# Optimization experiments

Measured on AMD Instinct MI355X. Metric: run time of the kernel, lower is better.

The kernel has to match this reference:

```python
import jax, jax.numpy as jnp
import numpy as np
import math

B, S, DIM = 2, 2048, 4096
N_HEADS, N_KV_HEADS = 32, 8
HEAD_DIM = DIM // N_HEADS  # 128
N_REP = N_HEADS // N_KV_HEADS  # 4
ROPE_THETA = 10000.0


def setup_inputs() -> dict:
    key = jax.random.key(0)
    ks = jax.random.split(key, 6)
    x = jax.random.normal(ks[0], (B, S, DIM), dtype=jnp.float32)
    wq = jax.random.normal(ks[1], (DIM, DIM), dtype=jnp.float32) * 0.02
    wk = jax.random.normal(ks[2], (N_KV_HEADS * HEAD_DIM, DIM), dtype=jnp.float32) * 0.02
    wv = jax.random.normal(ks[3], (N_KV_HEADS * HEAD_DIM, DIM), dtype=jnp.float32) * 0.02
    wo = jax.random.normal(ks[4], (DIM, DIM), dtype=jnp.float32) * 0.02
    # rotary freqs_cis (seqlen, head_dim//2), represented as cos/sin
    inv_freq = 1.0 / (ROPE_THETA ** (jnp.arange(0, HEAD_DIM, 2, dtype=jnp.float32) / HEAD_DIM))
    angles = jnp.arange(S, dtype=jnp.float32)[:, None] * inv_freq[None, :]  # [S, HEAD_DIM//2]
    freqs_cos = jnp.cos(angles)
    freqs_sin = jnp.sin(angles)
    # additive causal mask [S, S]: 0 on/below diagonal, -inf above
    mask = jnp.where(jnp.tril(jnp.ones((S, S), dtype=bool)), 0.0, -jnp.inf).astype(jnp.float32)
    return {"x": x, "wq": wq, "wk": wk, "wv": wv, "wo": wo,
            "freqs_cos": freqs_cos, "freqs_sin": freqs_sin, "mask": mask}


def _apply_rotary(t, freqs_cos, freqs_sin):
    # t: [B, S, H, HEAD_DIM]; interpret pairs (even, odd) as complex
    t2 = t.reshape(*t.shape[:-1], HEAD_DIM // 2, 2)
    tr, ti = t2[..., 0], t2[..., 1]
    c = freqs_cos[None, :, None, :]  # [1, S, 1, HD/2]
    s = freqs_sin[None, :, None, :]
    out_r = tr * c - ti * s
    out_i = tr * s + ti * c
    return jnp.stack([out_r, out_i], axis=-1).reshape(t.shape)


def reference(x, wq, wk, wv, wo, freqs_cos, freqs_sin, mask):
    bsz, seqlen, _ = x.shape
    xq = (x @ wq.T).reshape(bsz, seqlen, N_HEADS, HEAD_DIM)
    xk = (x @ wk.T).reshape(bsz, seqlen, N_KV_HEADS, HEAD_DIM)
    xv = (x @ wv.T).reshape(bsz, seqlen, N_KV_HEADS, HEAD_DIM)
    xq = _apply_rotary(xq, freqs_cos, freqs_sin)
    xk = _apply_rotary(xk, freqs_cos, freqs_sin)
    # repeat_kv (GQA): [B,S,KV,HD] -> [B,S,KV*N_REP,HD] via repeat_interleave on head axis
    keys = jnp.repeat(xk, N_REP, axis=2)
    values = jnp.repeat(xv, N_REP, axis=2)
    # scores: [B, H, S, S]
    scores = jnp.einsum('bqhd,bkhd->bhqk', xq, keys) / math.sqrt(HEAD_DIM)
    scores = scores + mask[None, None, :, :]
    probs = jax.nn.softmax(scores.astype(jnp.float32), axis=-1).astype(xq.dtype)
    out = jnp.einsum('bhqk,bkhd->bqhd', probs, values).reshape(bsz, seqlen, DIM)
    return out @ wo.T
```

## Files before the change

### kernel.cpp

```cpp
#include <hip/hip_runtime.h>

typedef __bf16 bf16;
typedef __bf16 bf16x4 __attribute__((ext_vector_type(4)));
typedef __bf16 bf16x8 __attribute__((ext_vector_type(8)));
typedef float f32x4 __attribute__((ext_vector_type(4)));

#define BB 2
#define SS 2048
#define DIM 4096
#define KVDIM 1024
#define NH 32
#define NKV 8
#define HD 128
#define NEGINF (-1e30f)

__device__ __forceinline__ void async16(void* lds, const void* gmem) {
    __builtin_amdgcn_global_load_lds(
        (const __attribute__((address_space(1))) void*)gmem,
        (__attribute__((address_space(3))) void*)lds, 16, 0, 0);
}

__device__ __forceinline__ f32x4 mfma16(bf16x8 a, bf16x8 b, f32x4 c) {
    return __builtin_amdgcn_mfma_f32_16x16x32_bf16(a, b, c, 0, 0, 0);
}

struct DetectArgs { const void* p[7]; int n[7]; };

__global__ void detect_dtypes(DetectArgs a, int* flags) {
    __shared__ int bad;
    const int ti = blockIdx.x;
    if (threadIdx.x == 0) bad = 0;
    __syncthreads();
    const bf16* s = (const bf16*)a.p[ti];
    int n = a.n[ti];
    int take = n < 8192 ? n : 8192;
    int lbad = 0;
    for (int i = threadIdx.x; i < take; i += 256) {
        float f = (float)s[i];
        if (!(f > -1e4f && f < 1e4f)) lbad = 1;
    }
    if (lbad) atomicOr(&bad, 1);
    __syncthreads();
    if (threadIdx.x == 0) flags[ti] = bad;
}

__device__ __forceinline__ void conv8(const void* src, bf16* dst, int rel, int flag) {
    if (flag) {
        const float* s = (const float*)src + (size_t)rel * 8;
        bf16x8 v;
#pragma unroll
        for (int j = 0; j < 8; ++j) v[j] = (bf16)s[j];
        *(bf16x8*)(dst + (size_t)rel * 8) = v;
    } else {
        *(bf16x8*)(dst + (size_t)rel * 8) = *((const bf16x8*)src + rel);
    }
}

__global__ void convert_to_bf16(const void* __restrict__ src, bf16* __restrict__ dst,
                                int n8, const int* __restrict__ flagp) {
    int i = blockIdx.x * 256 + threadIdx.x;
    if (i >= n8) return;
    conv8(src, dst, i, *flagp);
}

__global__ void convert4(const void* s0, bf16* d0, int n0, const int* f0,
                         const void* s1, bf16* d1, int n1, const int* f1,
                         const void* s2, bf16* d2, int n2, const int* f2,
                         const void* s3, bf16* d3, int n3, const int* f3) {
    int u = blockIdx.x * 256 + threadIdx.x;
    if (u < n0)                       { conv8(s0, d0, u, *f0); return; }
    u -= n0;
    if (u < n1)                       { conv8(s1, d1, u, *f1); return; }
    u -= n1;
    if (u < n2)                       { conv8(s2, d2, u, *f2); return; }
    u -= n2;
    if (u < n3)                       { conv8(s3, d3, u, *f3); return; }
}

#define SBAR()  asm volatile("s_barrier" ::: "memory")
#define LGKM0() asm volatile("s_waitcnt lgkmcnt(0)" ::: "memory")
#define VM8()   asm volatile("s_waitcnt vmcnt(8)" ::: "memory")
#define VM4()   asm volatile("s_waitcnt vmcnt(4)" ::: "memory")
#define VM0()   asm volatile("s_waitcnt vmcnt(0)" ::: "memory")

__device__ __forceinline__ void gemm256_core(const bf16* __restrict__ A,
                                             const bf16* __restrict__ B,
                                             int K, int m0, int n0,
                                             f32x4 (&acc)[8][4]) {
    __shared__ bf16 sm[2][4][8192];
    const int t = threadIdx.x;
    const int lane = t & 63;
    const int w = t >> 6;
    const int l15 = lane & 15, quad = lane >> 4;
    const int wm = w >> 2;
    const int wn = w & 3;
    const int axr = l15 & 7;
    const int c0 = (quad ^ axr) * 8;
    const int c1 = ((4 + quad) ^ axr) * 8;
    const int srl = t >> 3;
    const int sch = ((t & 7) ^ (srl & 7)) * 8;
    const size_t Ks = (size_t)K;

    bf16x8 aReg[4][2], bReg[4][2];

#define RD_A(c_, mh) { \
    const bf16* ab = &sm[c_][wm][0] + ((mh) * 64 + l15) * 64; \
    _Pragma("unroll") for (int i = 0; i < 4; ++i) { \
        aReg[i][0] = *(const bf16x8*)(ab + i * 1024 + c0); \
        aReg[i][1] = *(const bf16x8*)(ab + i * 1024 + c1); } }

#define RD_B(c_, nh) { \
    const bf16* bb = &sm[c_][2 + (wn >> 1)][0] + ((wn & 1) * 64 + (nh) * 32 + l15) * 64; \
    _Pragma("unroll") for (int jj = 0; jj < 2; ++jj) { \
        bReg[(nh) * 2 + jj][0] = *(const bf16x8*)(bb + jj * 1024 + c0); \
        bReg[(nh) * 2 + jj][1] = *(const bf16x8*)(bb + jj * 1024 + c1); } }

#define STG(c_, reg_, Mat, rowbase, kt) { \
    bf16* d_ = &sm[c_][reg_][0] + (size_t)t * 8; \
    const bf16* s_ = (Mat) + ((size_t)((rowbase) + srl)) * Ks + (size_t)(kt) * 64 + sch; \
    async16(d_, s_); \
    async16(d_ + 4096, s_ + 64 * Ks); }

#define MM(mh, nh) { \
    _Pragma("unroll") for (int i = 0; i < 4; ++i) \
    _Pragma("unroll") for (int jj = 0; jj < 2; ++jj) { \
        acc[(mh) * 4 + i][(nh) * 2 + jj] = \
            mfma16(aReg[i][0], bReg[(nh) * 2 + jj][0], acc[(mh) * 4 + i][(nh) * 2 + jj]); \
        acc[(mh) * 4 + i][(nh) * 2 + jj] = \
            mfma16(aReg[i][1], bReg[(nh) * 2 + jj][1], acc[(mh) * 4 + i][(nh) * 2 + jj]); } }

    STG(0, 0, A, m0, 0);
    STG(0, 2, B, n0, 0);
    STG(0, 1, A, m0 + 128, 0);
    STG(0, 3, B, n0 + 128, 0);
    STG(1, 2, B, n0, 1);
    STG(1, 0, A, m0, 1);
    VM4(); SBAR();

    const int NT = K >> 6;
    for (int T = 0; T < NT; ++T) {
        const int c = T & 1, nc = c ^ 1;
        const int kt1 = (T + 1 < NT) ? T + 1 : 0;
        const int kt2 = (T + 2 < NT) ? T + 2 : 0;
        RD_A(c, 0); RD_B(c, 0);
        STG(nc, 1, A, m0 + 128, kt1);
        SBAR();
        __builtin_amdgcn_s_setprio(1); MM(0, 0); __builtin_amdgcn_s_setprio(0);
        LGKM0(); SBAR();
        RD_B(c, 1);
        STG(nc, 3, B, n0 + 128, kt1);
        SBAR();
        __builtin_amdgcn_s_setprio(1); MM(0, 1); __builtin_amdgcn_s_setprio(0);
        LGKM0(); SBAR();
        RD_A(c, 1);
        STG(c, 2, B, n0, kt2);
        SBAR();
        __builtin_amdgcn_s_setprio(1); MM(1, 0); __builtin_amdgcn_s_setprio(0);
        LGKM0(); SBAR();
        STG(c, 0, A, m0, kt2);
        SBAR();
        __builtin_amdgcn_s_setprio(1); MM(1, 1); __builtin_amdgcn_s_setprio(0);
        LGKM0(); VM4(); SBAR();
    }
#undef RD_A
#undef RD_B
#undef STG
#undef MM
}

__global__ __launch_bounds__(512, 2)
void gemm_nt(const bf16* __restrict__ A, const bf16* __restrict__ B,
             bf16* __restrict__ C, int M, int N, int K) {
    const int t = threadIdx.x, lane = t & 63, w = t >> 6;
    const int l15 = lane & 15, quad = lane >> 4;
    const int wm = w >> 2, wn = w & 3;
    const int m0 = blockIdx.y * 256, n0 = blockIdx.x * 256;
    f32x4 acc[8][4] = {};
    gemm256_core(A, B, K, m0, n0, acc);
#pragma unroll
    for (int i = 0; i < 8; ++i)
#pragma unroll
        for (int j = 0; j < 4; ++j) {
            int col = n0 + wn * 64 + j * 16 + l15;
#pragma unroll
            for (int r = 0; r < 4; ++r)
                C[(size_t)(m0 + wm * 128 + i * 16 + quad * 4 + r) * N + col] = (bf16)acc[i][j][r];
        }
}

__global__ __launch_bounds__(512, 2)
void gemm_nt_kv(const bf16* __restrict__ A, const bf16* __restrict__ Bkv,
                bf16* __restrict__ Kc, bf16* __restrict__ Vc, int M, int K) {
    const int t = threadIdx.x, lane = t & 63, w = t >> 6;
    const int l15 = lane & 15, quad = lane >> 4;
    const int wm = w >> 2, wn = w & 3;
    const int m0 = blockIdx.y * 256, n0 = blockIdx.x * 256;
    f32x4 acc[8][4] = {};
    gemm256_core(A, Bkv, K, m0, n0, acc);
    bf16* C = (n0 < KVDIM) ? Kc : Vc;
    const int cb = (n0 < KVDIM) ? n0 : n0 - KVDIM;
#pragma unroll
    for (int i = 0; i < 8; ++i)
#pragma unroll
        for (int j = 0; j < 4; ++j) {
            int col = cb + wn * 64 + j * 16 + l15;
#pragma unroll
            for (int r = 0; r < 4; ++r)
                C[(size_t)(m0 + wm * 128 + i * 16 + quad * 4 + r) * KVDIM + col] = (bf16)acc[i][j][r];
        }
}

__global__ __launch_bounds__(512, 2)
void gemm_nt_out(const bf16* __restrict__ A, const bf16* __restrict__ B,
                 void* __restrict__ C, int M, int N, int K,
                 const int* __restrict__ flagp) {
    const int t = threadIdx.x, lane = t & 63, w = t >> 6;
    const int l15 = lane & 15, quad = lane >> 4;
    const int wm = w >> 2, wn = w & 3;
    const int m0 = blockIdx.y * 256, n0 = blockIdx.x * 256;
    const int f32out = *flagp;
    f32x4 acc[8][4] = {};
    gemm256_core(A, B, K, m0, n0, acc);
#pragma unroll
    for (int i = 0; i < 8; ++i)
#pragma unroll
        for (int j = 0; j < 4; ++j) {
            int col = n0 + wn * 64 + j * 16 + l15;
#pragma unroll
            for (int r = 0; r < 4; ++r) {
                int row = m0 + wm * 128 + i * 16 + quad * 4 + r;
                if (f32out) ((float*)C)[(size_t)row * N + col] = acc[i][j][r];
                else        ((bf16*)C)[(size_t)row * N + col] = (bf16)acc[i][j][r];
            }
        }
}

__device__ __forceinline__ void rope8(bf16* p, const bf16* fc, const bf16* fs,
                                      int s, int i0, float sc) {
    bf16x8 v = *(bf16x8*)p;
    bf16x8 o;
#pragma unroll
    for (int j = 0; j < 4; ++j) {
        float tr = (float)v[2 * j], ti = (float)v[2 * j + 1];
        float cc = (float)fc[s * 64 + i0 + j];
        float sn = (float)fs[s * 64 + i0 + j];
        o[2 * j]     = (bf16)((tr * cc - ti * sn) * sc);
        o[2 * j + 1] = (bf16)((tr * sn + ti * cc) * sc);
    }
    *(bf16x8*)p = o;
}

#define ROPE_BLOCKS ((DIM * (BB * SS) / 8 + KVDIM * (BB * SS) / 8) / 256)

__global__ void rope_tv(bf16* __restrict__ Q, bf16* __restrict__ Kr,
                        const bf16* __restrict__ fc, const bf16* __restrict__ fs,
                        const bf16* __restrict__ V, bf16* __restrict__ Vt) {
    __shared__ bf16 tile[64][74];
    const int bid = blockIdx.x;
    const int t = threadIdx.x;
    if (bid < ROPE_BLOCKS) {
        const float qscale = 0.08838834764831845f * 1.4426950408889634f;
        int u = bid * 256 + t;
        const int QU = (DIM * (BB * SS)) / 8;
        if (u < QU) {
            int row = u >> 9;
            int c = (u & 511) * 8;
            rope8(Q + (size_t)row * DIM + c, fc, fs, row & (SS - 1), (c >> 1) & 63, qscale);
        } else {
            u -= QU;
            int row = u >> 7;
            int c = (u & 127) * 8;
            rope8(Kr + (size_t)row * KVDIM + c, fc, fs, row & (SS - 1), (c >> 1) & 63, 1.0f);
        }
        return;
    }
    const int b2 = bid - ROPE_BLOCKS;
    const int st = b2 & 31, ct = (b2 >> 5) & 15, b = b2 >> 9;
    const int s0 = st * 64;
    const int kvh = ct >> 1, d0 = (ct & 1) * 64;
#pragma unroll
    for (int i = 0; i < 2; ++i) {
        int o = i * 256 + t;
        int r = o >> 3, c8 = (o & 7) * 8;
        bf16x8 v = *(const bf16x8*)(V + (size_t)(b * SS + s0 + r) * KVDIM + kvh * HD + d0 + c8);
#pragma unroll
        for (int j = 0; j < 8; ++j) tile[r][c8 + j] = v[j];
    }
    __syncthreads();
#pragma unroll
    for (int i = 0; i < 2; ++i) {
        int o = i * 256 + t;
        int sseg = (o & 7) * 8, dl = o >> 3;
        bf16x8 v;
#pragma unroll
        for (int j = 0; j < 8; ++j) v[j] = tile[sseg + j][dl];
        *(bf16x8*)(Vt + ((size_t)((b * NKV + kvh) * HD) + d0 + dl) * SS + s0 + sseg) = v;
    }
}

__global__ __launch_bounds__(256, 2)
void flash_attn(const bf16* __restrict__ Q, const bf16* __restrict__ Kr,
                const bf16* __restrict__ Vt, bf16* __restrict__ AO) {
    __shared__ char smem[49152];
    bf16* Vts = (bf16*)(smem + 32768);
    const int t = threadIdx.x, w = t >> 6, lane = t & 63;
    const int l15 = lane & 15, quad = lane >> 4;
    const int bh = blockIdx.x;
    const int b = bh >> 5, h = bh & 31, kvh = h >> 2;
    const int q0 = ((int)gridDim.y - 1 - (int)blockIdx.y) * 128;

#define STAGE_K(kb_, kk_) { \
    char* kbase_ = smem + (kb_) * 16384; \
    _Pragma("unroll") for (int i = 0; i < 4; ++i) { \
        int s_ = i * 256 + t; \
        int key_ = s_ >> 4, slot_ = s_ & 15; \
        int dseg_ = slot_ ^ (key_ & 15); \
        async16(kbase_ + (size_t)s_ * 16, \
                Kr + (size_t)(b * SS + (kk_) + key_) * KVDIM + kvh * HD + dseg_ * 8); } }
#define STAGE_V(kk_) { \
    _Pragma("unroll") for (int i = 0; i < 4; ++i) { \
        int s_ = i * 256 + t; \
        int d_ = s_ >> 3, slot_ = s_ & 7; \
        int kseg_ = slot_ ^ (d_ & 7); \
        async16((char*)Vts + (size_t)s_ * 16, \
                Vt + ((size_t)((b * NKV + kvh) * HD + d_)) * SS + (kk_) + kseg_ * 8); } }

    bf16x8 qf[2][4];
#pragma unroll
    for (int mi = 0; mi < 2; ++mi) {
        int qrow = b * SS + q0 + w * 32 + mi * 16 + l15;
#pragma unroll
        for (int ks = 0; ks < 4; ++ks)
            qf[mi][ks] = *(const bf16x8*)(Q + (size_t)qrow * DIM + h * HD + ks * 32 + quad * 8);
    }

    f32x4 of[2][8] = {};
    float mrow[2] = {NEGINF, NEGINF};
    float lrow[2] = {0.f, 0.f};

    const int nt = (q0 + 128) >> 6;
    STAGE_K(0, 0);
    for (int ti = 0; ti < nt; ++ti) {
        const int kk = ti << 6;
        const int cur = ti & 1, nxt = cur ^ 1;
        bf16* Ks = (bf16*)(smem + cur * 16384);
        char* Ps = smem + cur * 16384;
        STAGE_V(kk);
        STAGE_K(nxt, (ti + 1 < nt) ? kk + 64 : 0);
        VM8(); SBAR();

        f32x4 sacc[2][4] = {};
#pragma unroll
        for (int nt2 = 0; nt2 < 4; ++nt2) {
            int key = nt2 * 16 + l15;
#pragma unroll
            for (int ks = 0; ks < 4; ++ks) {
                int slot = (ks * 4 + quad) ^ (key & 15);
                bf16x8 kf = *(const bf16x8*)(Ks + key * 128 + slot * 8);
#pragma unroll
                for (int mi = 0; mi < 2; ++mi)
                    sacc[mi][nt2] = mfma16(kf, qf[mi][ks], sacc[mi][nt2]);
            }
        }
        if (kk >= q0) {
#pragma unroll
            for (int mi = 0; mi < 2; ++mi) {
                int q = q0 + w * 32 + mi * 16 + l15;
#pragma unroll
                for (int nt2 = 0; nt2 < 4; ++nt2) {
                    int kbase = kk + nt2 * 16 + quad * 4;
#pragma unroll
                    for (int r = 0; r < 4; ++r)
                        if (kbase + r > q) sacc[mi][nt2][r] = NEGINF;
                }
            }
        }
#pragma unroll
        for (int mi = 0; mi < 2; ++mi) {
            float m01[4];
#pragma unroll
            for (int nt2 = 0; nt2 < 4; ++nt2)
                m01[nt2] = fmaxf(fmaxf(sacc[mi][nt2][0], sacc[mi][nt2][1]),
                                 fmaxf(sacc[mi][nt2][2], sacc[mi][nt2][3]));
            float mx = fmaxf(fmaxf(m01[0], m01[1]), fmaxf(m01[2], m01[3]));
            mx = fmaxf(mx, __shfl_xor(mx, 16));
            mx = fmaxf(mx, __shfl_xor(mx, 32));
            if (__all(mx - mrow[mi] <= 8.0f)) {
                float rs[4];
#pragma unroll
                for (int nt2 = 0; nt2 < 4; ++nt2) {
                    rs[nt2] = 0.f;
#pragma unroll
                    for (int r = 0; r < 4; ++r) {
                        float p = exp2f(sacc[mi][nt2][r] - mrow[mi]);
                        sacc[mi][nt2][r] = p;
                        rs[nt2] += p;
                    }
                }
                float rsum = (rs[0] + rs[1]) + (rs[2] + rs[3]);
                rsum += __shfl_xor(rsum, 16);
                rsum += __shfl_xor(rsum, 32);
                lrow[mi] += rsum;
            } else {
                float mnew = fmaxf(mrow[mi], mx);
                float alpha = exp2f(mrow[mi] - mnew);
                float rs[4];
#pragma unroll
                for (int nt2 = 0; nt2 < 4; ++nt2) {
                    rs[nt2] = 0.f;
#pragma unroll
                    for (int r = 0; r < 4; ++r) {
                        float p = exp2f(sacc[mi][nt2][r] - mnew);
                        sacc[mi][nt2][r] = p;
                        rs[nt2] += p;
                    }
                }
                float rsum = (rs[0] + rs[1]) + (rs[2] + rs[3]);
                rsum += __shfl_xor(rsum, 16);
                rsum += __shfl_xor(rsum, 32);
                lrow[mi] = lrow[mi] * alpha + rsum;
                mrow[mi] = mnew;
#pragma unroll
                for (int dt = 0; dt < 8; ++dt)
#pragma unroll
                    for (int r = 0; r < 4; ++r) of[mi][dt][r] *= alpha;
            }
        }
        VM4(); SBAR();
#pragma unroll
        for (int mi = 0; mi < 2; ++mi) {
            int row = w * 32 + mi * 16 + l15;
#pragma unroll
            for (int nt2 = 0; nt2 < 4; ++nt2) {
                bf16x4 pv;
#pragma unroll
                for (int r = 0; r < 4; ++r) pv[r] = (bf16)sacc[mi][nt2][r];
                int cc = nt2 * 2 + (quad >> 1);
                *(bf16x4*)(Ps + row * 128 + ((cc ^ (row & 7)) * 16 + (quad & 1) * 8)) = pv;
            }
        }
#pragma unroll
        for (int kb = 0; kb < 2; ++kb) {
            bf16x8 pa[2];
#pragma unroll
            for (int mi = 0; mi < 2; ++mi) {
                int row = w * 32 + mi * 16 + l15;
                pa[mi] = *(const bf16x8*)(Ps + row * 128 + (((kb * 4 + quad) ^ (row & 7)) * 16));
            }
#pragma unroll
            for (int dt = 0; dt < 8; ++dt) {
                int d = dt * 16 + l15;
                int slot = (kb * 4 + quad) ^ (d & 7);
                bf16x8 vb = *(const bf16x8*)(Vts + d * 64 + slot * 8);
#pragma unroll
                for (int mi = 0; mi < 2; ++mi)
                    of[mi][dt] = mfma16(vb, pa[mi], of[mi][dt]);
            }
        }
        SBAR();
    }
    VM0(); SBAR();
#undef STAGE_K
#undef STAGE_V
    bf16* Os = (bf16*)smem;
#pragma unroll
    for (int mi = 0; mi < 2; ++mi) {
        float inv = 1.0f / lrow[mi];
        int row = w * 32 + mi * 16 + l15;
#pragma unroll
        for (int dt = 0; dt < 8; ++dt) {
            bf16x4 o4;
#pragma unroll
            for (int r = 0; r < 4; ++r) o4[r] = (bf16)(of[mi][dt][r] * inv);
            int s = dt * 2 + (quad >> 1);
            int slot = s ^ l15;
            *(bf16x4*)((char*)Os + row * 256 + slot * 16 + (quad & 1) * 8) = o4;
        }
    }
    __syncthreads();
#pragma unroll
    for (int i = 0; i < 8; ++i) {
        int flat = i * 256 + t;
        int ql = flat >> 4, s = flat & 15;
        bf16x8 v = *(const bf16x8*)((char*)Os + ql * 256 + (s ^ (ql & 15)) * 16);
        *(bf16x8*)(AO + (size_t)(b * SS + q0 + ql) * DIM + h * HD + s * 8) = v;
    }
}

extern "C" void kernel_launch(void* const* d_in, const int* in_sizes, int n_in,
                              void* d_out, int out_size, void* d_ws, size_t ws_size,
                              hipStream_t stream) {
    const size_t MD = (size_t)BB * SS * DIM;
    const size_t KV = (size_t)BB * SS * KVDIM;
    const size_t FC = (size_t)SS * (HD / 2);
    const int M = BB * SS;

    int* flags = (int*)d_ws;
    bf16* xb  = (bf16*)((char*)d_ws + 32);
    bf16* wb  = xb + MD;
    bf16* Q   = wb + MD;
    bf16* Kr  = Q + MD;
    bf16* Vw  = Kr + KV;
    bf16* Vt  = Vw + KV;
    bf16* fcb = Vt + KV;
    bf16* fsb = fcb + FC;

    DetectArgs da;
    for (int i = 0; i < 7; ++i) { da.p[i] = d_in[i]; da.n[i] = in_sizes[i]; }
    detect_dtypes<<<7, 256, 0, stream>>>(da, flags);

    dim3 blk(256);
    dim3 blk512(512);

    {
        int n0 = (int)(MD / 8), n1 = (int)(FC / 8), n2 = (int)(FC / 8), n3 = (int)(MD / 8);
        int nb = (n0 + n1 + n2 + n3 + 255) / 256;
        convert4<<<nb, blk, 0, stream>>>(d_in[0], xb, n0, flags + 0,
                                         d_in[5], fcb, n1, flags + 5,
                                         d_in[6], fsb, n2, flags + 6,
                                         d_in[1], wb, n3, flags + 1);
    }
    gemm_nt<<<dim3(DIM / 256, M / 256), blk512, 0, stream>>>(xb, wb, Q, M, DIM, DIM);

    {
        int n0 = (int)(KV / 8), n1 = (int)(KV / 8);
        int nb = (n0 + n1 + 255) / 256;
        convert4<<<nb, blk, 0, stream>>>(d_in[2], wb, n0, flags + 2,
                                         d_in[3], wb + KV, n1, flags + 3,
                                         nullptr, nullptr, 0, flags + 2,
                                         nullptr, nullptr, 0, flags + 2);
    }
    gemm_nt_kv<<<dim3(2 * KVDIM / 256, M / 256), blk512, 0, stream>>>(xb, wb, Kr, Vw, M, DIM);

    rope_tv<<<dim3(ROPE_BLOCKS + (SS / 64) * 16 * BB), blk, 0, stream>>>(Q, Kr, fcb, fsb, Vw, Vt);

    flash_attn<<<dim3(BB * NH, SS / 128), blk, 0, stream>>>(Q, Kr, Vt, xb);

    convert_to_bf16<<<(int)(MD / 8 / 256), blk, 0, stream>>>(d_in[4], wb, (int)(MD / 8), flags + 4);
    gemm_nt_out<<<dim3(DIM / 256, M / 256), blk512, 0, stream>>>(xb, wb, d_out, M, DIM, DIM, flags + 0);
}
```

Before: 727.7 us.

## Widen flash attention blocks to 256 queries with 8 waves sharing K/V tiles

The flash attention kernel now runs 512 threads over 256 query rows per block instead of 256 threads over 128 rows. Each K/V tile staged in LDS is therefore reused by twice as many waves, which halves global K/V traffic per query. K double-buffering is dropped: each iteration loads K and V, then waits before computing, so load latency is no longer hidden behind compute. A per-wave 'live' flag skips QK, softmax and PV work on tiles that lie entirely above the causal diagonal. The epilogue writes the output in two halves to fit LDS. Risks are exposed load latency, waves sitting idle at barriers on causal-edge tiles, and fewer blocks in the grid.

```diff
diff --git a/kernel.cpp b/kernel.cpp
--- a/kernel.cpp
+++ b/kernel.cpp
@@ -79,8 +79,8 @@
 
 #define SBAR()  asm volatile("s_barrier" ::: "memory")
 #define LGKM0() asm volatile("s_waitcnt lgkmcnt(0)" ::: "memory")
-#define VM8()   asm volatile("s_waitcnt vmcnt(8)" ::: "memory")
 #define VM4()   asm volatile("s_waitcnt vmcnt(4)" ::: "memory")
+#define VM2()   asm volatile("s_waitcnt vmcnt(2)" ::: "memory")
 #define VM0()   asm volatile("s_waitcnt vmcnt(0)" ::: "memory")
 
 __device__ __forceinline__ void gemm256_core(const bf16* __restrict__ A,
@@ -298,28 +298,30 @@
     }
 }
 
-__global__ __launch_bounds__(256, 2)
+__global__ __launch_bounds__(512, 2)
 void flash_attn(const bf16* __restrict__ Q, const bf16* __restrict__ Kr,
                 const bf16* __restrict__ Vt, bf16* __restrict__ AO) {
     __shared__ char smem[49152];
+    bf16* Ks  = (bf16*)smem;
+    char* Ps  = smem;
     bf16* Vts = (bf16*)(smem + 32768);
     const int t = threadIdx.x, w = t >> 6, lane = t & 63;
     const int l15 = lane & 15, quad = lane >> 4;
     const int bh = blockIdx.x;
     const int b = bh >> 5, h = bh & 31, kvh = h >> 2;
-    const int q0 = ((int)gridDim.y - 1 - (int)blockIdx.y) * 128;
-
-#define STAGE_K(kb_, kk_) { \
-    char* kbase_ = smem + (kb_) * 16384; \
-    _Pragma("unroll") for (int i = 0; i < 4; ++i) { \
-        int s_ = i * 256 + t; \
+    const int q0 = ((int)gridDim.y - 1 - (int)blockIdx.y) * 256;
+    const int qw = q0 + w * 32;
+
+#define STAGE_K(kk_) { \
+    _Pragma("unroll") for (int i = 0; i < 2; ++i) { \
+        int s_ = i * 512 + t; \
         int key_ = s_ >> 4, slot_ = s_ & 15; \
         int dseg_ = slot_ ^ (key_ & 15); \
-        async16(kbase_ + (size_t)s_ * 16, \
+        async16((char*)Ks + (size_t)s_ * 16, \
                 Kr + (size_t)(b * SS + (kk_) + key_) * KVDIM + kvh * HD + dseg_ * 8); } }
 #define STAGE_V(kk_) { \
-    _Pragma("unroll") for (int i = 0; i < 4; ++i) { \
-        int s_ = i * 256 + t; \
+    _Pragma("unroll") for (int i = 0; i < 2; ++i) { \
+        int s_ = i * 512 + t; \
         int d_ = s_ >> 3, slot_ = s_ & 7; \
         int kseg_ = slot_ ^ (d_ & 7); \
         async16((char*)Vts + (size_t)s_ * 16, \
@@ -328,7 +330,7 @@
     bf16x8 qf[2][4];
 #pragma unroll
     for (int mi = 0; mi < 2; ++mi) {
-        int qrow = b * SS + q0 + w * 32 + mi * 16 + l15;
+        int qrow = b * SS + qw + mi * 16 + l15;
 #pragma unroll
         for (int ks = 0; ks < 4; ++ks)
             qf[mi][ks] = *(const bf16x8*)(Q + (size_t)qrow * DIM + h * HD + ks * 32 + quad * 8);
@@ -338,152 +340,157 @@
     float mrow[2] = {NEGINF, NEGINF};
     float lrow[2] = {0.f, 0.f};
 
-    const int nt = (q0 + 128) >> 6;
-    STAGE_K(0, 0);
-    for (int ti = 0; ti < nt; ++ti) {
-        const int kk = ti << 6;
-        const int cur = ti & 1, nxt = cur ^ 1;
-        bf16* Ks = (bf16*)(smem + cur * 16384);
-        char* Ps = smem + cur * 16384;
+    const int kend = q0 + 256;
+    for (int kk = 0; kk < kend; kk += 64) {
+        STAGE_K(kk);
         STAGE_V(kk);
-        STAGE_K(nxt, (ti + 1 < nt) ? kk + 64 : 0);
-        VM8(); SBAR();
-
+        VM2(); SBAR();
+
+        const bool live = kk <= qw + 31;
         f32x4 sacc[2][4] = {};
-#pragma unroll
-        for (int nt2 = 0; nt2 < 4; ++nt2) {
-            int key = nt2 * 16 + l15;
-#pragma unroll
-            for (int ks = 0; ks < 4; ++ks) {
-                int slot = (ks * 4 + quad) ^ (key & 15);
-                bf16x8 kf = *(const bf16x8*)(Ks + key * 128 + slot * 8);
-#pragma unroll
-                for (int mi = 0; mi < 2; ++mi)
-                    sacc[mi][nt2] = mfma16(kf, qf[mi][ks], sacc[mi][nt2]);
-            }
-        }
-        if (kk >= q0) {
+        if (live) {
+#pragma unroll
+            for (int nt2 = 0; nt2 < 4; ++nt2) {
+                int key = nt2 * 16 + l15;
+#pragma unroll
+                for (int ks = 0; ks < 4; ++ks) {
+                    int slot = (ks * 4 + quad) ^ (key & 15);
+                    bf16x8 kf = *(const bf16x8*)(Ks + key * 128 + slot * 8);
+#pragma unroll
+                    for (int mi = 0; mi < 2; ++mi)
+                        sacc[mi][nt2] = mfma16(kf, qf[mi][ks], sacc[mi][nt2]);
+                }
+            }
+            if (kk + 64 > qw) {
+#pragma unroll
+                for (int mi = 0; mi < 2; ++mi) {
+                    int q = qw + mi * 16 + l15;
+#pragma unroll
+                    for (int nt2 = 0; nt2 < 4; ++nt2) {
+                        int kbase = kk + nt2 * 16 + quad * 4;
+#pragma unroll
+                        for (int r = 0; r < 4; ++r)
+                            if (kbase + r > q) sacc[mi][nt2][r] = NEGINF;
+                    }
+                }
+            }
 #pragma unroll
             for (int mi = 0; mi < 2; ++mi) {
-                int q = q0 + w * 32 + mi * 16 + l15;
-#pragma unroll
-                for (int nt2 = 0; nt2 < 4; ++nt2) {
-                    int kbase = kk + nt2 * 16 + quad * 4;
-#pragma unroll
-                    for (int r = 0; r < 4; ++r)
-                        if (kbase + r > q) sacc[mi][nt2][r] = NEGINF;
-                }
-            }
-        }
-#pragma unroll
-        for (int mi = 0; mi < 2; ++mi) {
-            float m01[4];
-#pragma unroll
-            for (int nt2 = 0; nt2 < 4; ++nt2)
-                m01[nt2] = fmaxf(fmaxf(sacc[mi][nt2][0], sacc[mi][nt2][1]),
-                                 fmaxf(sacc[mi][nt2][2], sacc[mi][nt2][3]));
-            float mx = fmaxf(fmaxf(m01[0], m01[1]), fmaxf(m01[2], m01[3]));
-            mx = fmaxf(mx, __shfl_xor(mx, 16));
-            mx = fmaxf(mx, __shfl_xor(mx, 32));
-            if (__all(mx - mrow[mi] <= 8.0f)) {
-                float rs[4];
-#pragma unroll
-                for (int nt2 = 0; nt2 < 4; ++nt2) {
-                    rs[nt2] = 0.f;
-#pragma unroll
-                    for (int r = 0; r < 4; ++r) {
-                        float p = exp2f(sacc[mi][nt2][r] - mrow[mi]);
-                        sacc[mi][nt2][r] = p;
-                        rs[nt2] += p;
+                float m01[4];
+#pragma unroll
+                for (int nt2 = 0; nt2 < 4; ++nt2)
+                    m01[nt2] = fmaxf(fmaxf(sacc[mi][nt2][0], sacc[mi][nt2][1]),
+                                     fmaxf(sacc[mi][nt2][2], sacc[mi][nt2][3]));
+                float mx = fmaxf(fmaxf(m01[0], m01[1]), fmaxf(m01[2], m01[3]));
+                mx = fmaxf(mx, __shfl_xor(mx, 16));
+                mx = fmaxf(mx, __shfl_xor(mx, 32));
+                if (__all(mx - mrow[mi] <= 8.0f)) {
+                    float rs[4];
+#pragma unroll
+                    for (int nt2 = 0; nt2 < 4; ++nt2) {
+                        rs[nt2] = 0.f;
+#pragma unroll
+                        for (int r = 0; r < 4; ++r) {
+                            float p = exp2f(sacc[mi][nt2][r] - mrow[mi]);
+                            sacc[mi][nt2][r] = p;
+                            rs[nt2] += p;
+                        }
                     }
-                }
-                float rsum = (rs[0] + rs[1]) + (rs[2] + rs[3]);
-                rsum += __shfl_xor(rsum, 16);
-                rsum += __shfl_xor(rsum, 32);
-                lrow[mi] += rsum;
-            } else {
-                float mnew = fmaxf(mrow[mi], mx);
-                float alpha = exp2f(mrow[mi] - mnew);
-                float rs[4];
-#pragma unroll
-                for (int nt2 = 0; nt2 < 4; ++nt2) {
-                    rs[nt2] = 0.f;
-#pragma unroll
-                    for (int r = 0; r < 4; ++r) {
-                        float p = exp2f(sacc[mi][nt2][r] - mnew);
-                        sacc[mi][nt2][r] = p;
-                        rs[nt2] += p;
+                    float rsum = (rs[0] + rs[1]) + (rs[2] + rs[3]);
+                    rsum += __shfl_xor(rsum, 16);
+                    rsum += __shfl_xor(rsum, 32);
+                    lrow[mi] += rsum;
+                } else {
+                    float mnew = fmaxf(mrow[mi], mx);
+                    float alpha = exp2f(mrow[mi] - mnew);
+                    float rs[4];
+#pragma unroll
+                    for (int nt2 = 0; nt2 < 4; ++nt2) {
+                        rs[nt2] = 0.f;
+#pragma unroll
+                        for (int r = 0; r < 4; ++r) {
+                            float p = exp2f(sacc[mi][nt2][r] - mnew);
+                            sacc[mi][nt2][r] = p;
+                            rs[nt2] += p;
+                        }
                     }
-                }
-                float rsum = (rs[0] + rs[1]) + (rs[2] + rs[3]);
-                rsum += __shfl_xor(rsum, 16);
-                rsum += __shfl_xor(rsum, 32);
-                lrow[mi] = lrow[mi] * alpha + rsum;
-                mrow[mi] = mnew;
-#pragma unroll
-                for (int dt = 0; dt < 8; ++dt)
-#pragma unroll
-                    for (int r = 0; r < 4; ++r) of[mi][dt][r] *= alpha;
-            }
-        }
-        VM4(); SBAR();
-#pragma unroll
-        for (int mi = 0; mi < 2; ++mi) {
-            int row = w * 32 + mi * 16 + l15;
-#pragma unroll
-            for (int nt2 = 0; nt2 < 4; ++nt2) {
-                bf16x4 pv;
-#pragma unroll
-                for (int r = 0; r < 4; ++r) pv[r] = (bf16)sacc[mi][nt2][r];
-                int cc = nt2 * 2 + (quad >> 1);
-                *(bf16x4*)(Ps + row * 128 + ((cc ^ (row & 7)) * 16 + (quad & 1) * 8)) = pv;
-            }
-        }
-#pragma unroll
-        for (int kb = 0; kb < 2; ++kb) {
-            bf16x8 pa[2];
+                    float rsum = (rs[0] + rs[1]) + (rs[2] + rs[3]);
+                    rsum += __shfl_xor(rsum, 16);
+                    rsum += __shfl_xor(rsum, 32);
+                    lrow[mi] = lrow[mi] * alpha + rsum;
+                    mrow[mi] = mnew;
+#pragma unroll
+                    for (int dt = 0; dt < 8; ++dt)
+#pragma unroll
+                        for (int r = 0; r < 4; ++r) of[mi][dt][r] *= alpha;
+                }
+            }
+        }
+        VM0(); SBAR();
+        if (live) {
 #pragma unroll
             for (int mi = 0; mi < 2; ++mi) {
                 int row = w * 32 + mi * 16 + l15;
-                pa[mi] = *(const bf16x8*)(Ps + row * 128 + (((kb * 4 + quad) ^ (row & 7)) * 16));
-            }
-#pragma unroll
-            for (int dt = 0; dt < 8; ++dt) {
-                int d = dt * 16 + l15;
-                int slot = (kb * 4 + quad) ^ (d & 7);
-                bf16x8 vb = *(const bf16x8*)(Vts + d * 64 + slot * 8);
-#pragma unroll
-                for (int mi = 0; mi < 2; ++mi)
-                    of[mi][dt] = mfma16(vb, pa[mi], of[mi][dt]);
+#pragma unroll
+                for (int nt2 = 0; nt2 < 4; ++nt2) {
+                    bf16x4 pv;
+#pragma unroll
+                    for (int r = 0; r < 4; ++r) pv[r] = (bf16)sacc[mi][nt2][r];
+                    int cc = nt2 * 2 + (quad >> 1);
+                    *(bf16x4*)(Ps + row * 128 + ((cc ^ (row & 7)) * 16 + (quad & 1) * 8)) = pv;
+                }
+            }
+#pragma unroll
+            for (int kb = 0; kb < 2; ++kb) {
+                bf16x8 pa[2];
+#pragma unroll
+                for (int mi = 0; mi < 2; ++mi) {
+                    int row = w * 32 + mi * 16 + l15;
+                    pa[mi] = *(const bf16x8*)(Ps + row * 128 + (((kb * 4 + quad) ^ (row & 7)) * 16));
+                }
+#pragma unroll
+                for (int dt = 0; dt < 8; ++dt) {
+                    int d = dt * 16 + l15;
+                    int slot = (kb * 4 + quad) ^ (d & 7);
+                    bf16x8 vb = *(const bf16x8*)(Vts + d * 64 + slot * 8);
+#pragma unroll
+                    for (int mi = 0; mi < 2; ++mi)
+                        of[mi][dt] = mfma16(vb, pa[mi], of[mi][dt]);
+                }
             }
         }
         SBAR();
     }
-    VM0(); SBAR();
 #undef STAGE_K
 #undef STAGE_V
     bf16* Os = (bf16*)smem;
 #pragma unroll
-    for (int mi = 0; mi < 2; ++mi) {
-        float inv = 1.0f / lrow[mi];
-        int row = w * 32 + mi * 16 + l15;
-#pragma unroll
-        for (int dt = 0; dt < 8; ++dt) {
-            bf16x4 o4;
-#pragma unroll
-            for (int r = 0; r < 4; ++r) o4[r] = (bf16)(of[mi][dt][r] * inv);
-            int s = dt * 2 + (quad >> 1);
-            int slot = s ^ l15;
-            *(bf16x4*)((char*)Os + row * 256 + slot * 16 + (quad & 1) * 8) = o4;
-        }
-    }
-    __syncthreads();
-#pragma unroll
-    for (int i = 0; i < 8; ++i) {
-        int flat = i * 256 + t;
-        int ql = flat >> 4, s = flat & 15;
-        bf16x8 v = *(const bf16x8*)((char*)Os + ql * 256 + (s ^ (ql & 15)) * 16);
-        *(bf16x8*)(AO + (size_t)(b * SS + q0 + ql) * DIM + h * HD + s * 8) = v;
+    for (int half = 0; half < 2; ++half) {
+        __syncthreads();
+        if ((w >> 2) == half) {
+#pragma unroll
+            for (int mi = 0; mi < 2; ++mi) {
+                float inv = 1.0f / lrow[mi];
+                int row = (w & 3) * 32 + mi * 16 + l15;
+#pragma unroll
+                for (int dt = 0; dt < 8; ++dt) {
+                    bf16x4 o4;
+#pragma unroll
+                    for (int r = 0; r < 4; ++r) o4[r] = (bf16)(of[mi][dt][r] * inv);
+                    int s = dt * 2 + (quad >> 1);
+                    int slot = s ^ l15;
+                    *(bf16x4*)((char*)Os + row * 256 + slot * 16 + (quad & 1) * 8) = o4;
+                }
+            }
+        }
+        __syncthreads();
+#pragma unroll
+        for (int i = 0; i < 4; ++i) {
+            int flat = i * 512 + t;
+            int ql = flat >> 4, s = flat & 15;
+            bf16x8 v = *(const bf16x8*)((char*)Os + ql * 256 + (s ^ (ql & 15)) * 16);
+            *(bf16x8*)(AO + (size_t)(b * SS + q0 + half * 128 + ql) * DIM + h * HD + s * 8) = v;
+        }
     }
 }
 
@@ -534,7 +541,7 @@
 
     rope_tv<<<dim3(ROPE_BLOCKS + (SS / 64) * 16 * BB), blk, 0, stream>>>(Q, Kr, fcb, fsb, Vw, Vt);
 
-    flash_attn<<<dim3(BB * NH, SS / 128), blk, 0, stream>>>(Q, Kr, Vt, xb);
+    flash_attn<<<dim3(BB * NH, SS / 256), blk512, 0, stream>>>(Q, Kr, Vt, xb);
 
     convert_to_bf16<<<(int)(MD / 8 / 256), blk, 0, stream>>>(d_in[4], wb, (int)(MD / 8), flags + 4);
     gemm_nt_out<<<dim3(DIM / 256, M / 256), blk512, 0, stream>>>(xb, wb, d_out, M, DIM, DIM, flags + 0);
```

After: 745.1 us. 1.02x slower.
